# Performance work log

Measured on AMD Instinct MI355X. Metric: run time of the kernel, lower is better.

The kernel has to match this reference:

```python
import jax, jax.numpy as jnp
import numpy as np

B, S, V, D = 64, 256, 50000, 300
NW, CL, CV, CD = 8192, 16, 500, 30
H, T, CH = 128, 17, 30


def setup_inputs() -> dict:
    key = jax.random.key(0)
    ks = jax.random.split(key, 32)
    f32 = jnp.float32
    def rn(k, shape, scale=0.1):
        return jax.random.normal(k, shape, dtype=f32) * scale
    inp = {}
    inp["char_emb"] = rn(ks[0], (CV, CD)).at[0].set(0.0)  # padding_idx=0
    inp["conv_w"] = rn(ks[1], (CH, CD, 3))  # OIH
    inp["conv_b"] = rn(ks[2], (CH,))
    inp["word_emb"] = rn(ks[3], (V, D))
    in0, in1 = D + CH, 2 * H
    inp["w_ih_l0"] = rn(ks[4], (2, 3 * H, in0))  # [dir, 3H, in]
    inp["w_hh_l0"] = rn(ks[5], (2, 3 * H, H))
    inp["b_ih_l0"] = rn(ks[6], (2, 3 * H))
    inp["b_hh_l0"] = rn(ks[7], (2, 3 * H))
    inp["w_ih_l1"] = rn(ks[8], (2, 3 * H, in1))
    inp["w_hh_l1"] = rn(ks[9], (2, 3 * H, H))
    inp["b_ih_l1"] = rn(ks[10], (2, 3 * H))
    inp["b_hh_l1"] = rn(ks[11], (2, 3 * H))
    inp["mlp_w1"] = rn(ks[12], (2 * H, H))
    inp["mlp_b1"] = rn(ks[13], (H,))
    inp["mlp_w2"] = rn(ks[14], (H, T))
    inp["mlp_b2"] = rn(ks[15], (T,))
    inp["crf_start"] = rn(ks[16], (T,))
    inp["crf_end"] = rn(ks[17], (T,))
    inp["crf_trans"] = rn(ks[18], (T, T))
    inp["batched_char_words"] = jax.random.randint(ks[19], (NW, CL), 0, CV)
    inp["batched_char_words_len"] = jax.random.randint(ks[20], (NW,), 1, CL + 1)
    inp["batched_char_word_index"] = jax.random.randint(ks[21], (B, S), 0, NW + 1)
    inp["batched_tokens"] = jax.random.randint(ks[22], (B, S), 0, V)
    inp["batched_tokens_len"] = jax.random.randint(ks[23], (B,), S // 2, S + 1)
    inp["target"] = jax.random.randint(ks[24], (B, S), 0, T)
    return inp


def _gru_dir(x, mask, w_ih, w_hh, b_ih, b_hh, reverse):
    # x: [B,S,I], mask: [B,S] bool. Masked (padded) steps carry hidden state
    # through unchanged, matching pack_padded_sequence semantics.
    xg = jnp.einsum('bsi,gi->sbg', x, w_ih) + b_ih  # [S,B,3H]
    m = mask.T  # [S,B]
    h0 = jnp.zeros((x.shape[0], w_hh.shape[1]), x.dtype)

    def step(h, inp):
        xt, mt = inp
        hg = h @ w_hh.T + b_hh
        xr, xz, xn = jnp.split(xt, 3, axis=-1)
        hr, hz, hn = jnp.split(hg, 3, axis=-1)
        r = jax.nn.sigmoid(xr + hr)
        z = jax.nn.sigmoid(xz + hz)
        n = jnp.tanh(xn + r * hn)
        hnew = (1.0 - z) * n + z * h
        h = jnp.where(mt[:, None], hnew, h)
        return h, h

    _, hs = jax.lax.scan(step, h0, (xg, m), reverse=reverse)
    return hs.transpose(1, 0, 2)  # [B,S,H]


def _bigru_layer(x, mask, w_ih, w_hh, b_ih, b_hh):
    fwd = _gru_dir(x, mask, w_ih[0], w_hh[0], b_ih[0], b_hh[0], False)
    bwd = _gru_dir(x, mask, w_ih[1], w_hh[1], b_ih[1], b_hh[1], True)
    return jnp.concatenate([fwd, bwd], axis=-1)


def _forward(char_emb, conv_w, conv_b, word_emb,
             w_ih_l0, w_hh_l0, b_ih_l0, b_hh_l0,
             w_ih_l1, w_hh_l1, b_ih_l1, b_hh_l1,
             mlp_w1, mlp_b1, mlp_w2, mlp_b2,
             crf_start, crf_end, crf_trans,
             batched_char_words, batched_char_word_index,
             batched_tokens, batched_tokens_len, target):
    # --- char CNN token encoder: conv1d(k=3, SAME) + relu + max-over-time ---
    ct = char_emb[batched_char_words]  # [NW,CL,CD]
    c = jax.lax.conv_general_dilated(ct.transpose(0, 2, 1), conv_w, (1,), 'SAME',
                                     dimension_numbers=('NCH', 'OIH', 'NCH'))
    c = jax.nn.relu(c + conv_b[None, :, None])
    tok_enc = jnp.max(c, axis=-1)  # [NW,CH]
    tok_enc = jnp.concatenate([jnp.zeros((1, tok_enc.shape[1]), tok_enc.dtype), tok_enc], axis=0)
    tok_idx = tok_enc[batched_char_word_index]  # [B,S,CH] (index 0 -> zeros)

    texts = jnp.concatenate([word_emb[batched_tokens], tok_idx], axis=-1)  # [B,S,D+CH]
    seq = batched_tokens.shape[1]
    mask = jnp.arange(seq)[None, :] < batched_tokens_len[:, None]  # [B,S]

    # --- 2-layer BiGRU ---
    h = _bigru_layer(texts, mask, w_ih_l0, w_hh_l0, b_ih_l0, b_hh_l0)
    h = _bigru_layer(h, mask, w_ih_l1, w_hh_l1, b_ih_l1, b_hh_l1)

    # --- MLP head -> emissions [B,S,17] ---
    h = jax.nn.relu(h @ mlp_w1 + mlp_b1)
    emissions = h @ mlp_w2 + mlp_b2

    # --- CRF negative log-likelihood, reduction='token_mean' ---
    maskf = mask.astype(emissions.dtype)
    emit_sc = jnp.take_along_axis(emissions, target[..., None], axis=-1)[..., 0]  # [B,S]
    trans_sc = crf_trans[target[:, :-1], target[:, 1:]]  # [B,S-1]
    score = crf_start[target[:, 0]] + emit_sc[:, 0]
    score = score + jnp.sum((trans_sc + emit_sc[:, 1:]) * maskf[:, 1:], axis=1)
    last_tags = jnp.take_along_axis(target, (batched_tokens_len - 1)[:, None], axis=1)[:, 0]
    score = score + crf_end[last_tags]

    alpha0 = crf_start[None, :] + emissions[:, 0]  # [B,T]
    em_rest = emissions[:, 1:].transpose(1, 0, 2)  # [S-1,B,T]
    m_rest = mask[:, 1:].T  # [S-1,B]

    def crf_step(alpha, inp):
        emit, mt = inp
        new = jax.nn.logsumexp(alpha[:, :, None] + crf_trans[None], axis=1) + emit
        return jnp.where(mt[:, None], new, alpha), None

    alpha, _ = jax.lax.scan(crf_step, alpha0, (em_rest, m_rest))
    log_z = jax.nn.logsumexp(alpha + crf_end[None, :], axis=1)
    llh = score - log_z
    return -(jnp.sum(llh) / jnp.sum(maskf))


def reference(char_emb, conv_w, conv_b, word_emb,
              w_ih_l0, w_hh_l0, b_ih_l0, b_hh_l0,
              w_ih_l1, w_hh_l1, b_ih_l1, b_hh_l1,
              mlp_w1, mlp_b1, mlp_w2, mlp_b2,
              crf_start, crf_end, crf_trans,
              batched_char_words, batched_char_words_len,
              batched_char_word_index, batched_tokens, batched_tokens_len, target):
    return _forward(char_emb, conv_w, conv_b, word_emb,
                    w_ih_l0, w_hh_l0, b_ih_l0, b_hh_l0,
                    w_ih_l1, w_hh_l1, b_ih_l1, b_hh_l1,
                    mlp_w1, mlp_b1, mlp_w2, mlp_b2,
                    crf_start, crf_end, crf_trans,
                    batched_char_words, batched_char_word_index,
                    batched_tokens, batched_tokens_len, target)
```

## Files before the change

kernel.cpp:

```cpp
#include <hip/hip_runtime.h>
#include <cstddef>

#define BATCH 64
#define SEQ   256
#define VOCAB 50000
#define DIM   300
#define NW    8192
#define CLEN  16
#define CDIM  30
#define CHC   30
#define HID   128
#define NT    17
#define IN0   (DIM + CHC)
#define IN0P  336
#define IN1   (2 * HID)
#define NPOS  (BATCH * SEQ)

constexpr size_t SZ_XG    = 2ull * BATCH * SEQ * 384;
constexpr size_t SZ_TEXTS = (size_t)NPOS * IN0P;
constexpr size_t SZ_H1    = (size_t)NPOS * 256;
constexpr size_t SZ_TOK   = 245792;
constexpr size_t SZ_EMIS  = (size_t)NPOS * NT;
constexpr size_t SZ_WPAD  = 768ull * IN0P;
constexpr size_t OFF_XG    = 0;
constexpr size_t OFF_TEXTS = OFF_XG + SZ_XG;
constexpr size_t OFF_H1    = OFF_TEXTS + SZ_TEXTS;
constexpr size_t OFF_TOK   = OFF_H1 + SZ_H1;
constexpr size_t OFF_EMIS  = OFF_TOK + SZ_TOK;
constexpr size_t OFF_WPAD  = OFF_EMIS + SZ_EMIS;
constexpr size_t OFF_LLH   = OFF_WPAD + SZ_WPAD;

__device__ __forceinline__ float sigm(float x) {
    return 1.f / (1.f + __expf(-x));
}
__device__ __forceinline__ float tanh_fast(float x) {
    x = fminf(fmaxf(x, -15.f), 15.f);
    float e = __expf(-2.f * x);
    return (1.f - e) / (1.f + e);
}

__global__ __launch_bounds__(256) void char_conv_k(
    const float* __restrict__ char_emb,
    const float* __restrict__ conv_w,
    const float* __restrict__ conv_b,
    const int*   __restrict__ words,
    float* __restrict__ tok_enc)
{
    __shared__ __align__(16) float cs[8][CLEN][CDIM];
    __shared__ float wsm[CHC * CDIM * 3];
    __shared__ float bs[CHC];
    int n0 = blockIdx.x * 8;
    int tid = threadIdx.x;
    for (int e = tid; e < CHC * CDIM * 3; e += 256) wsm[e] = conv_w[e];
    if (tid < CHC) bs[tid] = conv_b[tid];
    for (int e = tid; e < 8 * CLEN * CDIM; e += 256) {
        int wi = e / (CLEN * CDIM);
        int rem = e - wi * (CLEN * CDIM);
        int l = rem / CDIM;
        int i = rem - l * CDIM;
        int ci = words[(n0 + wi) * CLEN + l];
        cs[wi][l][i] = char_emb[ci * CDIM + i];
    }
    __syncthreads();
    int wi = tid >> 5;
    int o = tid & 31;
    if (o < CHC) {
        float best = -1e30f;
        for (int l = 0; l < CLEN; l++) {
            float s = 0.f;
            #pragma unroll
            for (int k = 0; k < 3; k++) {
                int ll = l + k - 1;
                if (ll >= 0 && ll < CLEN) {
                    #pragma unroll
                    for (int i = 0; i < CDIM; i++)
                        s += cs[wi][ll][i] * wsm[(o * CDIM + i) * 3 + k];
                }
            }
            best = fmaxf(best, s);
        }
        tok_enc[(size_t)(n0 + wi + 1) * CDIM + o] = fmaxf(best + bs[o], 0.f);
    }
}

__global__ __launch_bounds__(128) void build_texts_k(
    const float* __restrict__ word_emb,
    const float* __restrict__ tok_enc,
    const int*   __restrict__ tokens,
    const int*   __restrict__ widx,
    float* __restrict__ texts)
{
    int p = blockIdx.x;
    int tok = tokens[p];
    int ci = widx[p];
    float* o = texts + (size_t)p * IN0P;
    const float* wr = word_emb + (size_t)tok * DIM;
    const float* tr = tok_enc + (size_t)ci * CDIM;
    for (int c = threadIdx.x; c < IN0P; c += 128)
        o[c] = (c < DIM) ? wr[c] : (c < IN0 ? tr[c - DIM] : 0.f);
}

__global__ __launch_bounds__(64) void pad_w_k(
    const float* __restrict__ w, float* __restrict__ wp)
{
    int r = blockIdx.x;
    for (int c = threadIdx.x; c < IN0P; c += 64)
        wp[(size_t)r * IN0P + c] = (c < IN0) ? w[(size_t)r * IN0 + c] : 0.f;
}

#define GBM 128
#define GBN 128
#define GBK 16
__global__ __launch_bounds__(256) void gemm_xg_k(
    const float* __restrict__ A,
    const float* __restrict__ W,
    const float* __restrict__ bias,
    float* __restrict__ out,
    int K)
{
    __shared__ __align__(16) float As[GBK][GBM];
    __shared__ __align__(16) float Ws[GBK][GBN];
    int tid = threadIdx.x;
    int m0 = blockIdx.x * GBM;
    int n0 = blockIdx.y * GBN;
    int lrow = tid >> 1;
    int lk = (tid & 1) * 8;
    int ty = tid >> 4;
    int tx = tid & 15;

    float acc[8][8];
    #pragma unroll
    for (int i = 0; i < 8; i++)
        #pragma unroll
        for (int j = 0; j < 8; j++) acc[i][j] = 0.f;

    for (int k0 = 0; k0 < K; k0 += GBK) {
        const float4* ap = (const float4*)(A + (size_t)(m0 + lrow) * K + k0 + lk);
        const float4* wp = (const float4*)(W + (size_t)(n0 + lrow) * K + k0 + lk);
        float4 va0 = ap[0], va1 = ap[1];
        float4 vw0 = wp[0], vw1 = wp[1];
        As[lk + 0][lrow] = va0.x; As[lk + 1][lrow] = va0.y;
        As[lk + 2][lrow] = va0.z; As[lk + 3][lrow] = va0.w;
        As[lk + 4][lrow] = va1.x; As[lk + 5][lrow] = va1.y;
        As[lk + 6][lrow] = va1.z; As[lk + 7][lrow] = va1.w;
        Ws[lk + 0][lrow] = vw0.x; Ws[lk + 1][lrow] = vw0.y;
        Ws[lk + 2][lrow] = vw0.z; Ws[lk + 3][lrow] = vw0.w;
        Ws[lk + 4][lrow] = vw1.x; Ws[lk + 5][lrow] = vw1.y;
        Ws[lk + 6][lrow] = vw1.z; Ws[lk + 7][lrow] = vw1.w;
        __syncthreads();
        #pragma unroll
        for (int k = 0; k < GBK; k++) {
            float4 a0 = *(const float4*)&As[k][ty * 8];
            float4 a1 = *(const float4*)&As[k][ty * 8 + 4];
            float4 b0 = *(const float4*)&Ws[k][tx * 8];
            float4 b1 = *(const float4*)&Ws[k][tx * 8 + 4];
            float av[8] = {a0.x, a0.y, a0.z, a0.w, a1.x, a1.y, a1.z, a1.w};
            float bv[8] = {b0.x, b0.y, b0.z, b0.w, b1.x, b1.y, b1.z, b1.w};
            #pragma unroll
            for (int i = 0; i < 8; i++)
                #pragma unroll
                for (int j = 0; j < 8; j++)
                    acc[i][j] += av[i] * bv[j];
        }
        __syncthreads();
    }
    int nb = n0 + tx * 8;
    int d = nb / 384;
    int g0 = nb - d * 384;
    float bvv[8];
    #pragma unroll
    for (int j = 0; j < 8; j++) bvv[j] = bias[nb + j];
    int mbase = m0 + ty * 8;
    #pragma unroll
    for (int i = 0; i < 8; i++) {
        int m = mbase + i;
        int b = m >> 8;
        int t = m & 255;
        float* op = out + (((size_t)(d * BATCH + b) * SEQ + t) * 384 + g0);
        #pragma unroll
        for (int j = 0; j < 8; j++) op[j] = acc[i][j] + bvv[j];
    }
}

__global__ __launch_bounds__(512, 1) void gru_rec_k(
    const float* __restrict__ xg,
    const float* __restrict__ w_hh,
    const float* __restrict__ b_hh,
    const int*   __restrict__ lens,
    float* __restrict__ out)
{
    int d = blockIdx.x & 1;
    int b = blockIdx.x >> 1;
    int i = threadIdx.x;
    int e = i >> 2;
    int c = i & 3;
    __shared__ __align__(16) float hS[2 * HID];

    int rR = e, rZ = HID + e, rN = 2 * HID + e;
    const float* wbase = w_hh + (size_t)d * 384 * HID;
    float4 wR[8], wZ[8], wN[8];
    {
        const float4* pR = (const float4*)(wbase + (size_t)rR * HID + 32 * c);
        const float4* pZ = (const float4*)(wbase + (size_t)rZ * HID + 32 * c);
        const float4* pN = (const float4*)(wbase + (size_t)rN * HID + 32 * c);
        #pragma unroll
        for (int q = 0; q < 8; q++) { wR[q] = pR[q]; wZ[q] = pZ[q]; wN[q] = pN[q]; }
    }
    float bhR = b_hh[d * 384 + rR];
    float bhZ = b_hh[d * 384 + rZ];
    float bhN = b_hh[d * 384 + rN];
    int len = lens[b];

    if (i < HID) hS[i] = 0.f;
    float hold = 0.f;
    __syncthreads();

    const float* xgb = xg + ((size_t)(d * BATCH + b)) * SEQ * 384;
    float* outb = out + (size_t)b * SEQ * 256 + d * HID;

    int t0 = d ? (SEQ - 1) : 0;
    float xvR = xgb[(size_t)t0 * 384 + rR];
    float xvZ = xgb[(size_t)t0 * 384 + rZ];
    float xvN = xgb[(size_t)t0 * 384 + rN];

    for (int s = 0; s < SEQ; s++) {
        int t = d ? (SEQ - 1 - s) : s;
        int sn = (s + 1 < SEQ) ? (s + 1) : s;
        int tn = d ? (SEQ - 1 - sn) : sn;
        float nxvR = xgb[(size_t)tn * 384 + rR];
        float nxvZ = xgb[(size_t)tn * 384 + rZ];
        float nxvN = xgb[(size_t)tn * 384 + rN];

        const float4* h4 = (const float4*)(hS + (s & 1) * HID) + c * 8;
        float sR0 = 0.f, sR1 = 0.f, sZ0 = 0.f, sZ1 = 0.f, sN0 = 0.f, sN1 = 0.f;
        #pragma unroll
        for (int q = 0; q < 4; q++) {
            float4 x = h4[q];
            sR0 += wR[q].x * x.x + wR[q].y * x.y + wR[q].z * x.z + wR[q].w * x.w;
            sZ0 += wZ[q].x * x.x + wZ[q].y * x.y + wZ[q].z * x.z + wZ[q].w * x.w;
            sN0 += wN[q].x * x.x + wN[q].y * x.y + wN[q].z * x.z + wN[q].w * x.w;
        }
        #pragma unroll
        for (int q = 4; q < 8; q++) {
            float4 x = h4[q];
            sR1 += wR[q].x * x.x + wR[q].y * x.y + wR[q].z * x.z + wR[q].w * x.w;
            sZ1 += wZ[q].x * x.x + wZ[q].y * x.y + wZ[q].z * x.z + wZ[q].w * x.w;
            sN1 += wN[q].x * x.x + wN[q].y * x.y + wN[q].z * x.z + wN[q].w * x.w;
        }
        float sR = sR0 + sR1, sZ = sZ0 + sZ1, sN = sN0 + sN1;
        sR += __shfl_xor(sR, 1, 64); sR += __shfl_xor(sR, 2, 64);
        sZ += __shfl_xor(sZ, 1, 64); sZ += __shfl_xor(sZ, 2, 64);
        sN += __shfl_xor(sN, 1, 64); sN += __shfl_xor(sN, 2, 64);

        float r = sigm(xvR + sR + bhR);
        float z = sigm(xvZ + sZ + bhZ);
        float n = tanh_fast(xvN + r * (sN + bhN));
        float hnew = (1.f - z) * n + z * hold;
        hold = (t < len) ? hnew : hold;
        if (c == 0) {
            hS[((s & 1) ^ 1) * HID + e] = hold;
            outb[(size_t)t * 256 + e] = hold;
        }
        __syncthreads();
        xvR = nxvR; xvZ = nxvZ; xvN = nxvN;
    }
}

__global__ __launch_bounds__(128) void mlp_emis_k(
    const float* __restrict__ h1,
    const float* __restrict__ w1,
    const float* __restrict__ b1,
    const float* __restrict__ w2,
    const float* __restrict__ b2,
    float* __restrict__ emis)
{
    __shared__ __align__(16) float hrow[8 * 256];
    __shared__ float hid[8][HID];
    int p0 = blockIdx.x * 8;
    int tid = threadIdx.x;
    for (int e = tid; e < 8 * 256; e += 128)
        hrow[e] = h1[(size_t)p0 * 256 + e];
    __syncthreads();
    float acc[8];
    float bb = b1[tid];
    #pragma unroll
    for (int i = 0; i < 8; i++) acc[i] = bb;
    for (int k = 0; k < 256; k++) {
        float wv = w1[k * HID + tid];
        #pragma unroll
        for (int i = 0; i < 8; i++) acc[i] += hrow[i * 256 + k] * wv;
    }
    #pragma unroll
    for (int i = 0; i < 8; i++) hid[i][tid] = fmaxf(acc[i], 0.f);
    __syncthreads();
    for (int idx = tid; idx < 8 * NT; idx += 128) {
        int pos = idx / NT;
        int tg = idx - pos * NT;
        float a = b2[tg];
        for (int k = 0; k < HID; k++) a += hid[pos][k] * w2[k * NT + tg];
        emis[(size_t)(p0 + pos) * NT + tg] = a;
    }
}

__global__ __launch_bounds__(64) void crf_k(
    const float* __restrict__ emis,
    const float* __restrict__ start,
    const float* __restrict__ endv,
    const float* __restrict__ trans,
    const int*   __restrict__ target,
    const int*   __restrict__ lens,
    float* __restrict__ llh)
{
    int b = blockIdx.x;
    int tid = threadIdx.x;
    __shared__ float tr[NT * NT];
    __shared__ float aSh[NT];
    __shared__ float scoreSh;
    for (int e = tid; e < NT * NT; e += 64) tr[e] = trans[e];
    __syncthreads();
    int len = lens[b];
    const int* tgt = target + b * SEQ;
    const float* eb = emis + (size_t)b * SEQ * NT;

    float part = 0.f;
    for (int t = 1 + tid; t < SEQ; t += 64) {
        if (t < len) {
            int tp = tgt[t - 1], tc = tgt[t];
            part += tr[tp * NT + tc] + eb[(size_t)t * NT + tc];
        }
    }
    #pragma unroll
    for (int off = 32; off > 0; off >>= 1)
        part += __shfl_down(part, off, 64);
    if (tid == 0) {
        int t0 = tgt[0];
        scoreSh = part + start[t0] + eb[t0] + endv[tgt[len - 1]];
    }

    float a = (tid < NT) ? (start[tid] + eb[tid]) : 0.f;
    for (int t = 1; t < SEQ; t++) {
        if (tid < NT) aSh[tid] = a;
        __syncthreads();
        if (t < len && tid < NT) {
            float m = -1e30f;
            #pragma unroll
            for (int i = 0; i < NT; i++)
                m = fmaxf(m, aSh[i] + tr[i * NT + tid]);
            float ssum = 0.f;
            #pragma unroll
            for (int i = 0; i < NT; i++)
                ssum += __expf(aSh[i] + tr[i * NT + tid] - m);
            a = m + __logf(ssum) + eb[(size_t)t * NT + tid];
        }
        __syncthreads();
    }
    float v = (tid < NT) ? (a + endv[tid]) : -1e30f;
    float m = v;
    #pragma unroll
    for (int off = 32; off > 0; off >>= 1)
        m = fmaxf(m, __shfl_down(m, off, 64));
    m = __shfl(m, 0, 64);
    float e = (tid < NT) ? __expf(v - m) : 0.f;
    #pragma unroll
    for (int off = 32; off > 0; off >>= 1)
        e += __shfl_down(e, off, 64);
    if (tid == 0) {
        float logz = m + __logf(e);
        llh[b] = scoreSh - logz;
    }
}

__global__ __launch_bounds__(64) void finalize_k(
    const float* __restrict__ llh,
    const int*   __restrict__ lens,
    float* __restrict__ out)
{
    int tid = threadIdx.x;
    float s = llh[tid];
    float lf = (float)lens[tid];
    #pragma unroll
    for (int off = 32; off > 0; off >>= 1) {
        s += __shfl_down(s, off, 64);
        lf += __shfl_down(lf, off, 64);
    }
    if (tid == 0) out[0] = -(s / lf);
}

extern "C" void kernel_launch(void* const* d_in, const int* in_sizes, int n_in,
                              void* d_out, int out_size, void* d_ws, size_t ws_size,
                              hipStream_t stream) {
    const float* char_emb = (const float*)d_in[0];
    const float* conv_w   = (const float*)d_in[1];
    const float* conv_b   = (const float*)d_in[2];
    const float* word_emb = (const float*)d_in[3];
    const float* w_ih_l0  = (const float*)d_in[4];
    const float* w_hh_l0  = (const float*)d_in[5];
    const float* b_ih_l0  = (const float*)d_in[6];
    const float* b_hh_l0  = (const float*)d_in[7];
    const float* w_ih_l1  = (const float*)d_in[8];
    const float* w_hh_l1  = (const float*)d_in[9];
    const float* b_ih_l1  = (const float*)d_in[10];
    const float* b_hh_l1  = (const float*)d_in[11];
    const float* mlp_w1   = (const float*)d_in[12];
    const float* mlp_b1   = (const float*)d_in[13];
    const float* mlp_w2   = (const float*)d_in[14];
    const float* mlp_b2   = (const float*)d_in[15];
    const float* crf_start= (const float*)d_in[16];
    const float* crf_end  = (const float*)d_in[17];
    const float* crf_trans= (const float*)d_in[18];
    const int* bcw   = (const int*)d_in[19];
    const int* bcwi  = (const int*)d_in[21];
    const int* btok  = (const int*)d_in[22];
    const int* blen  = (const int*)d_in[23];
    const int* target= (const int*)d_in[24];

    float* ws    = (float*)d_ws;
    float* xg    = ws + OFF_XG;
    float* texts = ws + OFF_TEXTS;
    float* h0    = texts;
    float* h1    = ws + OFF_H1;
    float* tok   = ws + OFF_TOK;
    float* emis  = ws + OFF_EMIS;
    float* wpad  = ws + OFF_WPAD;
    float* llh   = ws + OFF_LLH;

    hipMemsetAsync(tok, 0, CDIM * sizeof(float), stream);
    pad_w_k<<<768, 64, 0, stream>>>(w_ih_l0, wpad);
    char_conv_k<<<NW / 8, 256, 0, stream>>>(char_emb, conv_w, conv_b, bcw, tok);
    build_texts_k<<<NPOS, 128, 0, stream>>>(word_emb, tok, btok, bcwi, texts);
    gemm_xg_k<<<dim3(NPOS / GBM, 768 / GBN), 256, 0, stream>>>(texts, wpad, b_ih_l0, xg, IN0P);
    gru_rec_k<<<2 * BATCH, 512, 0, stream>>>(xg, w_hh_l0, b_hh_l0, blen, h0);
    gemm_xg_k<<<dim3(NPOS / GBM, 768 / GBN), 256, 0, stream>>>(h0, w_ih_l1, b_ih_l1, xg, IN1);
    gru_rec_k<<<2 * BATCH, 512, 0, stream>>>(xg, w_hh_l1, b_hh_l1, blen, h1);
    mlp_emis_k<<<NPOS / 8, 128, 0, stream>>>(h1, mlp_w1, mlp_b1, mlp_w2, mlp_b2, emis);
    crf_k<<<BATCH, 64, 0, stream>>>(emis, crf_start, crf_end, crf_trans, target, blen, llh);
    finalize_k<<<1, 64, 0, stream>>>(llh, blen, (float*)d_out);
}
```

Before: 1.055 ms.

## Tune GRU recurrence: DPP quad reductions, rotated smem reads, deferred output stores

Changes the sequential GRU recurrence kernel in four ways. The quad-lane reductions use DPP instead of shuffles. The hidden-state reads are rotated per lane so the four lanes of a quad hit different shared-memory banks. The global store of the hidden state is moved to the next iteration so it sits outside the barrier critical path. Launch bounds now allow two blocks per CU. The aim is lower per-step latency in the serial loop, at the cost of a register budget that could cause spills under the tighter launch bound.

```diff
diff --git a/kernel.cpp b/kernel.cpp
--- a/kernel.cpp
+++ b/kernel.cpp
@@ -37,6 +37,13 @@
     x = fminf(fmaxf(x, -15.f), 15.f);
     float e = __expf(-2.f * x);
     return (1.f - e) / (1.f + e);
+}
+__device__ __forceinline__ float quad_sum(float x) {
+    int y = __builtin_amdgcn_update_dpp(0, __float_as_int(x), 0xB1, 0xF, 0xF, false);
+    x += __int_as_float(y);
+    y = __builtin_amdgcn_update_dpp(0, __float_as_int(x), 0x4E, 0xF, 0xF, false);
+    x += __int_as_float(y);
+    return x;
 }
 
 __global__ __launch_bounds__(256) void char_conv_k(
@@ -182,7 +189,7 @@
     }
 }
 
-__global__ __launch_bounds__(512, 1) void gru_rec_k(
+__global__ __launch_bounds__(512, 2) void gru_rec_k(
     const float* __restrict__ xg,
     const float* __restrict__ w_hh,
     const float* __restrict__ b_hh,
@@ -194,24 +201,26 @@
     int i = threadIdx.x;
     int e = i >> 2;
     int c = i & 3;
-    __shared__ __align__(16) float hS[2 * HID];
+    __shared__ __align__(16) float hS[2][HID];
 
     int rR = e, rZ = HID + e, rN = 2 * HID + e;
-    const float* wbase = w_hh + (size_t)d * 384 * HID;
+    const float* wbR = w_hh + ((size_t)d * 384 + rR) * HID + 32 * c;
+    const float* wbZ = w_hh + ((size_t)d * 384 + rZ) * HID + 32 * c;
+    const float* wbN = w_hh + ((size_t)d * 384 + rN) * HID + 32 * c;
     float4 wR[8], wZ[8], wN[8];
-    {
-        const float4* pR = (const float4*)(wbase + (size_t)rR * HID + 32 * c);
-        const float4* pZ = (const float4*)(wbase + (size_t)rZ * HID + 32 * c);
-        const float4* pN = (const float4*)(wbase + (size_t)rN * HID + 32 * c);
-        #pragma unroll
-        for (int q = 0; q < 8; q++) { wR[q] = pR[q]; wZ[q] = pZ[q]; wN[q] = pN[q]; }
+    #pragma unroll
+    for (int q = 0; q < 8; q++) {
+        int m = (q + c) & 7;
+        wR[q] = *(const float4*)(wbR + 4 * m);
+        wZ[q] = *(const float4*)(wbZ + 4 * m);
+        wN[q] = *(const float4*)(wbN + 4 * m);
     }
     float bhR = b_hh[d * 384 + rR];
     float bhZ = b_hh[d * 384 + rZ];
     float bhN = b_hh[d * 384 + rN];
     int len = lens[b];
 
-    if (i < HID) hS[i] = 0.f;
+    if (i < HID) { hS[0][i] = 0.f; }
     float hold = 0.f;
     __syncthreads();
 
@@ -222,48 +231,42 @@
     float xvR = xgb[(size_t)t0 * 384 + rR];
     float xvZ = xgb[(size_t)t0 * 384 + rZ];
     float xvN = xgb[(size_t)t0 * 384 + rN];
+    int tPrev = 0;
 
     for (int s = 0; s < SEQ; s++) {
         int t = d ? (SEQ - 1 - s) : s;
+        if (s && c == 0) outb[(size_t)tPrev * 256 + e] = hold;
         int sn = (s + 1 < SEQ) ? (s + 1) : s;
         int tn = d ? (SEQ - 1 - sn) : sn;
         float nxvR = xgb[(size_t)tn * 384 + rR];
         float nxvZ = xgb[(size_t)tn * 384 + rZ];
         float nxvN = xgb[(size_t)tn * 384 + rN];
 
-        const float4* h4 = (const float4*)(hS + (s & 1) * HID) + c * 8;
-        float sR0 = 0.f, sR1 = 0.f, sZ0 = 0.f, sZ1 = 0.f, sN0 = 0.f, sN1 = 0.f;
+        const float4* hb = (const float4*)hS[s & 1] + 8 * c;
+        float sR = 0.f, sZ = 0.f, sN = 0.f;
         #pragma unroll
-        for (int q = 0; q < 4; q++) {
-            float4 x = h4[q];
-            sR0 += wR[q].x * x.x + wR[q].y * x.y + wR[q].z * x.z + wR[q].w * x.w;
-            sZ0 += wZ[q].x * x.x + wZ[q].y * x.y + wZ[q].z * x.z + wZ[q].w * x.w;
-            sN0 += wN[q].x * x.x + wN[q].y * x.y + wN[q].z * x.z + wN[q].w * x.w;
+        for (int q = 0; q < 8; q++) {
+            int m = (q + c) & 7;
+            float4 hv = hb[m];
+            sR += wR[q].x * hv.x + wR[q].y * hv.y + wR[q].z * hv.z + wR[q].w * hv.w;
+            sZ += wZ[q].x * hv.x + wZ[q].y * hv.y + wZ[q].z * hv.z + wZ[q].w * hv.w;
+            sN += wN[q].x * hv.x + wN[q].y * hv.y + wN[q].z * hv.z + wN[q].w * hv.w;
         }
-        #pragma unroll
-        for (int q = 4; q < 8; q++) {
-            float4 x = h4[q];
-            sR1 += wR[q].x * x.x + wR[q].y * x.y + wR[q].z * x.z + wR[q].w * x.w;
-            sZ1 += wZ[q].x * x.x + wZ[q].y * x.y + wZ[q].z * x.z + wZ[q].w * x.w;
-            sN1 += wN[q].x * x.x + wN[q].y * x.y + wN[q].z * x.z + wN[q].w * x.w;
-        }
-        float sR = sR0 + sR1, sZ = sZ0 + sZ1, sN = sN0 + sN1;
-        sR += __shfl_xor(sR, 1, 64); sR += __shfl_xor(sR, 2, 64);
-        sZ += __shfl_xor(sZ, 1, 64); sZ += __shfl_xor(sZ, 2, 64);
-        sN += __shfl_xor(sN, 1, 64); sN += __shfl_xor(sN, 2, 64);
+        sR = quad_sum(sR);
+        sZ = quad_sum(sZ);
+        sN = quad_sum(sN);
 
         float r = sigm(xvR + sR + bhR);
         float z = sigm(xvZ + sZ + bhZ);
         float n = tanh_fast(xvN + r * (sN + bhN));
         float hnew = (1.f - z) * n + z * hold;
         hold = (t < len) ? hnew : hold;
-        if (c == 0) {
-            hS[((s & 1) ^ 1) * HID + e] = hold;
-            outb[(size_t)t * 256 + e] = hold;
-        }
+        if (c == 0) hS[(s & 1) ^ 1][e] = hold;
+        tPrev = t;
+        xvR = nxvR; xvZ = nxvZ; xvN = nxvN;
         __syncthreads();
-        xvR = nxvR; xvZ = nxvZ; xvN = nxvN;
-    }
+    }
+    if (c == 0) outb[(size_t)tPrev * 256 + e] = hold;
 }
 
 __global__ __launch_bounds__(128) void mlp_emis_k(
```

Result: faster. 879.5 us (-16.6%).
